# Kernel optimization log

Hardware: AMD Instinct MI355X
Metric: run time of the kernel (lower is better)

Reference implementation:

```python
import jax, jax.numpy as jnp
import numpy as np
from jax import lax

N_FEATURES = 160
HIDDEN = 128
NUM_LAYERS = 2
BATCH = 256
SEQ = 512


def _lstm_layer(x, h0, c0, W_ih, W_hh, b_ih, b_hh):
    """Single LSTM layer, batch_first input x: [B, T, D]. Returns hs: [B, T, H].
    PyTorch gate order: i, f, g, o."""
    b = b_ih + b_hh  # [4H]

    def step(carry, xt):
        h, c = carry
        gates = xt @ W_ih.T + h @ W_hh.T + b  # [B, 4H]
        i, f, g, o = jnp.split(gates, 4, axis=-1)
        i = jax.nn.sigmoid(i)
        f = jax.nn.sigmoid(f)
        g = jnp.tanh(g)
        o = jax.nn.sigmoid(o)
        c = f * c + i * g
        h = o * jnp.tanh(c)
        return (h, c), h

    xs = jnp.swapaxes(x, 0, 1)  # [T, B, D]
    (_, _), hs = lax.scan(step, (h0, c0), xs)
    return jnp.swapaxes(hs, 0, 1)  # [B, T, H]


def setup_inputs() -> dict:
    key = jax.random.key(0)
    ks = jax.random.split(key, 9)
    s = 1.0 / np.sqrt(HIDDEN)  # PyTorch LSTM init scale
    x = jax.random.normal(ks[0], (BATCH, SEQ, N_FEATURES), dtype=jnp.float32)
    h0 = jnp.zeros((NUM_LAYERS, BATCH, HIDDEN), dtype=jnp.float32)
    c0 = jnp.zeros((NUM_LAYERS, BATCH, HIDDEN), dtype=jnp.float32)
    return {
        "x": x,
        "h0": h0,
        "c0": c0,
        "W_ih0": jax.random.uniform(ks[1], (4 * HIDDEN, N_FEATURES), jnp.float32, -s, s),
        "W_hh0": jax.random.uniform(ks[2], (4 * HIDDEN, HIDDEN), jnp.float32, -s, s),
        "b_ih0": jax.random.uniform(ks[3], (4 * HIDDEN,), jnp.float32, -s, s),
        "b_hh0": jax.random.uniform(ks[4], (4 * HIDDEN,), jnp.float32, -s, s),
        "W_ih1": jax.random.uniform(ks[5], (4 * HIDDEN, HIDDEN), jnp.float32, -s, s),
        "W_hh1": jax.random.uniform(ks[6], (4 * HIDDEN, HIDDEN), jnp.float32, -s, s),
        "b_ih1": jax.random.uniform(ks[7], (4 * HIDDEN,), jnp.float32, -s, s),
        "b_hh1": jax.random.uniform(ks[8], (4 * HIDDEN,), jnp.float32, -s, s),
    }


def reference(x, h0, c0, W_ih0, W_hh0, b_ih0, b_hh0, W_ih1, W_hh1, b_ih1, b_hh1):
    h1 = _lstm_layer(x, h0[0], c0[0], W_ih0, W_hh0, b_ih0, b_hh0)   # [B, T, H]
    h2 = _lstm_layer(h1, h0[1], c0[1], W_ih1, W_hh1, b_ih1, b_hh1)  # [B, T, H]
    return h2[:, -1:, :]  # [B, 1, H]
```

## Files before the change

kernel.cpp:

```cpp
#include <hip/hip_runtime.h>


typedef _Float16 half2_t __attribute__((ext_vector_type(2)));

#define TSTEPS 512
#define HID 128

static __device__ __forceinline__ unsigned pack2(float a, float b) {
  half2_t h; h[0] = (_Float16)a; h[1] = (_Float16)b;
  return __builtin_bit_cast(unsigned, h);
}

static __device__ __forceinline__ float dot2f(unsigned a, unsigned b, float c) {
#if __has_builtin(__builtin_amdgcn_fdot2)
  return __builtin_amdgcn_fdot2(__builtin_bit_cast(half2_t, a),
                                __builtin_bit_cast(half2_t, b), c, false);
#else
  half2_t x = __builtin_bit_cast(half2_t, a);
  half2_t y = __builtin_bit_cast(half2_t, b);
  float r = c;
  r = fmaf((float)x[0], (float)y[0], r);
  r = fmaf((float)x[1], (float)y[1], r);
  return r;
#endif
}

static __device__ __forceinline__ float fast_rcp(float x) {
#if __has_builtin(__builtin_amdgcn_rcpf)
  return __builtin_amdgcn_rcpf(x);
#else
  return 1.0f / x;
#endif
}
static __device__ __forceinline__ float fast_exp2(float x) {
#if __has_builtin(__builtin_amdgcn_exp2f)
  return __builtin_amdgcn_exp2f(x);
#else
  return exp2f(x);
#endif
}
static __device__ __forceinline__ float sigm(float x) {
  return fast_rcp(1.0f + fast_exp2(x * -1.44269504f));
}
static __device__ __forceinline__ float tanh_f(float x) {
  float e = fast_exp2(x * 2.885390082f);
  return 1.0f - 2.0f * fast_rcp(e + 1.0f);
}

template <int CTRL>
static __device__ __forceinline__ float qp_add(float v) {
  int iv = __builtin_bit_cast(int, v);
  int t = __builtin_amdgcn_update_dpp(iv, iv, CTRL, 0xF, 0xF, true);
  return v + __builtin_bit_cast(float, t);
}

__global__ __launch_bounds__(512) __attribute__((amdgpu_waves_per_eu(1, 1)))
void lstm_fused(
    const float* __restrict__ x,
    const float* __restrict__ h0,
    const float* __restrict__ c0,
    const float* __restrict__ Wih0,
    const float* __restrict__ Whh0,
    const float* __restrict__ bih0, const float* __restrict__ bhh0,
    const float* __restrict__ Wih1,
    const float* __restrict__ Whh1,
    const float* __restrict__ bih1, const float* __restrict__ bhh1,
    float* __restrict__ out)
{
  const int b   = blockIdx.x;
  const int tid = threadIdx.x;
  const int c   = tid >> 2;
  const int s   = tid & 3;

  __shared__ unsigned h1s[TSTEPS][64];
  __shared__ unsigned xbuf[2][80];
  __shared__ unsigned h0buf[64];
  __shared__ unsigned hbuf[2][64];

  {
    unsigned wx[4][20], wh[4][16];
    float bias[4];
#pragma unroll
    for (int g = 0; g < 4; ++g) {
      const int r = g * HID + c;
#pragma unroll
      for (int j = 0; j < 20; ++j) {
        int p = 20 * s + j;
        wx[g][j] = pack2(Wih0[r * 160 + 2 * p], Wih0[r * 160 + 2 * p + 1]);
      }
#pragma unroll
      for (int j = 0; j < 16; ++j) {
        int p = 16 * s + j;
        wh[g][j] = pack2(Whh0[r * HID + 2 * p], Whh0[r * HID + 2 * p + 1]);
      }
      bias[g] = bih0[r] + bhh0[r];
    }

    float cst = c0[b * HID + c];

    if (tid < 64) h0buf[tid] = pack2(h0[b * HID + 2 * tid], h0[b * HID + 2 * tid + 1]);
    if (tid < 80) {
      float2 v = *(const float2*)&x[((size_t)b * TSTEPS + 0) * 160 + 2 * tid];
      xbuf[0][tid] = pack2(v.x, v.y);
    }
    float2 xA = make_float2(0.f, 0.f);
    if (tid < 80) xA = *(const float2*)&x[((size_t)b * TSTEPS + 1) * 160 + 2 * tid];
    __syncthreads();

#pragma unroll 1
    for (int t = 0; t < TSTEPS; ++t) {
      float2 xB = xA;
      if (tid < 80) {
        int tn = (t + 2 < TSTEPS) ? t + 2 : TSTEPS - 1;
        xB = *(const float2*)&x[((size_t)b * TSTEPS + tn) * 160 + 2 * tid];
      }

      const uint4* xs = (const uint4*)&xbuf[t & 1][20 * s];
      const uint4* hs = (t == 0) ? (const uint4*)&h0buf[16 * s]
                                 : (const uint4*)&h1s[t - 1][16 * s];
      float ai = 0.f, af = 0.f, ag = 0.f, ao = 0.f;
#pragma unroll
      for (int k = 0; k < 5; ++k) {
        uint4 v = xs[k];
        ai = dot2f(v.x, wx[0][4 * k + 0], ai); ai = dot2f(v.y, wx[0][4 * k + 1], ai);
        ai = dot2f(v.z, wx[0][4 * k + 2], ai); ai = dot2f(v.w, wx[0][4 * k + 3], ai);
        af = dot2f(v.x, wx[1][4 * k + 0], af); af = dot2f(v.y, wx[1][4 * k + 1], af);
        af = dot2f(v.z, wx[1][4 * k + 2], af); af = dot2f(v.w, wx[1][4 * k + 3], af);
        ag = dot2f(v.x, wx[2][4 * k + 0], ag); ag = dot2f(v.y, wx[2][4 * k + 1], ag);
        ag = dot2f(v.z, wx[2][4 * k + 2], ag); ag = dot2f(v.w, wx[2][4 * k + 3], ag);
        ao = dot2f(v.x, wx[3][4 * k + 0], ao); ao = dot2f(v.y, wx[3][4 * k + 1], ao);
        ao = dot2f(v.z, wx[3][4 * k + 2], ao); ao = dot2f(v.w, wx[3][4 * k + 3], ao);
      }
#pragma unroll
      for (int k = 0; k < 4; ++k) {
        uint4 v = hs[k];
        ai = dot2f(v.x, wh[0][4 * k + 0], ai); ai = dot2f(v.y, wh[0][4 * k + 1], ai);
        ai = dot2f(v.z, wh[0][4 * k + 2], ai); ai = dot2f(v.w, wh[0][4 * k + 3], ai);
        af = dot2f(v.x, wh[1][4 * k + 0], af); af = dot2f(v.y, wh[1][4 * k + 1], af);
        af = dot2f(v.z, wh[1][4 * k + 2], af); af = dot2f(v.w, wh[1][4 * k + 3], af);
        ag = dot2f(v.x, wh[2][4 * k + 0], ag); ag = dot2f(v.y, wh[2][4 * k + 1], ag);
        ag = dot2f(v.z, wh[2][4 * k + 2], ag); ag = dot2f(v.w, wh[2][4 * k + 3], ag);
        ao = dot2f(v.x, wh[3][4 * k + 0], ao); ao = dot2f(v.y, wh[3][4 * k + 1], ao);
        ao = dot2f(v.z, wh[3][4 * k + 2], ao); ao = dot2f(v.w, wh[3][4 * k + 3], ao);
      }
      ai = qp_add<0xB1>(ai); ai = qp_add<0x4E>(ai);
      af = qp_add<0xB1>(af); af = qp_add<0x4E>(af);
      ag = qp_add<0xB1>(ag); ag = qp_add<0x4E>(ag);
      ao = qp_add<0xB1>(ao); ao = qp_add<0x4E>(ao);

      float iv = sigm(ai + bias[0]);
      float fv = sigm(af + bias[1]);
      float gv = tanh_f(ag + bias[2]);
      float ov = sigm(ao + bias[3]);
      cst = fv * cst + iv * gv;
      float h = ov * tanh_f(cst);

      if (s == 0) ((_Float16*)h1s)[t * HID + c] = (_Float16)h;
      if (tid < 80) xbuf[(t + 1) & 1][tid] = pack2(xA.x, xA.y);
      __syncthreads();
      xA = xB;
    }
  }

  {
    unsigned w1x[4][16], w1h[4][16];
    float bias[4];
#pragma unroll
    for (int g = 0; g < 4; ++g) {
      const int r = g * HID + c;
#pragma unroll
      for (int j = 0; j < 16; ++j) {
        int p = 16 * s + j;
        w1x[g][j] = pack2(Wih1[r * HID + 2 * p], Wih1[r * HID + 2 * p + 1]);
        w1h[g][j] = pack2(Whh1[r * HID + 2 * p], Whh1[r * HID + 2 * p + 1]);
      }
      bias[g] = bih1[r] + bhh1[r];
    }

    const float* h0b = h0 + 256 * HID;
    const float* c0b = c0 + 256 * HID;
    float cst = c0b[b * HID + c];
    if (tid < 64) hbuf[0][tid] = pack2(h0b[b * HID + 2 * tid], h0b[b * HID + 2 * tid + 1]);
    __syncthreads();

    float hlast = 0.f;
#pragma unroll 1
    for (int t = 0; t < TSTEPS; ++t) {
      const uint4* xs = (const uint4*)&h1s[t][16 * s];
      const uint4* hs = (const uint4*)&hbuf[t & 1][16 * s];
      float ai = 0.f, af = 0.f, ag = 0.f, ao = 0.f;
#pragma unroll
      for (int k = 0; k < 4; ++k) {
        uint4 v = xs[k];
        ai = dot2f(v.x, w1x[0][4 * k + 0], ai); ai = dot2f(v.y, w1x[0][4 * k + 1], ai);
        ai = dot2f(v.z, w1x[0][4 * k + 2], ai); ai = dot2f(v.w, w1x[0][4 * k + 3], ai);
        af = dot2f(v.x, w1x[1][4 * k + 0], af); af = dot2f(v.y, w1x[1][4 * k + 1], af);
        af = dot2f(v.z, w1x[1][4 * k + 2], af); af = dot2f(v.w, w1x[1][4 * k + 3], af);
        ag = dot2f(v.x, w1x[2][4 * k + 0], ag); ag = dot2f(v.y, w1x[2][4 * k + 1], ag);
        ag = dot2f(v.z, w1x[2][4 * k + 2], ag); ag = dot2f(v.w, w1x[2][4 * k + 3], ag);
        ao = dot2f(v.x, w1x[3][4 * k + 0], ao); ao = dot2f(v.y, w1x[3][4 * k + 1], ao);
        ao = dot2f(v.z, w1x[3][4 * k + 2], ao); ao = dot2f(v.w, w1x[3][4 * k + 3], ao);
      }
#pragma unroll
      for (int k = 0; k < 4; ++k) {
        uint4 v = hs[k];
        ai = dot2f(v.x, w1h[0][4 * k + 0], ai); ai = dot2f(v.y, w1h[0][4 * k + 1], ai);
        ai = dot2f(v.z, w1h[0][4 * k + 2], ai); ai = dot2f(v.w, w1h[0][4 * k + 3], ai);
        af = dot2f(v.x, w1h[1][4 * k + 0], af); af = dot2f(v.y, w1h[1][4 * k + 1], af);
        af = dot2f(v.z, w1h[1][4 * k + 2], af); af = dot2f(v.w, w1h[1][4 * k + 3], af);
        ag = dot2f(v.x, w1h[2][4 * k + 0], ag); ag = dot2f(v.y, w1h[2][4 * k + 1], ag);
        ag = dot2f(v.z, w1h[2][4 * k + 2], ag); ag = dot2f(v.w, w1h[2][4 * k + 3], ag);
        ao = dot2f(v.x, w1h[3][4 * k + 0], ao); ao = dot2f(v.y, w1h[3][4 * k + 1], ao);
        ao = dot2f(v.z, w1h[3][4 * k + 2], ao); ao = dot2f(v.w, w1h[3][4 * k + 3], ao);
      }
      ai = qp_add<0xB1>(ai); ai = qp_add<0x4E>(ai);
      af = qp_add<0xB1>(af); af = qp_add<0x4E>(af);
      ag = qp_add<0xB1>(ag); ag = qp_add<0x4E>(ag);
      ao = qp_add<0xB1>(ao); ao = qp_add<0x4E>(ao);

      float iv = sigm(ai + bias[0]);
      float fv = sigm(af + bias[1]);
      float gv = tanh_f(ag + bias[2]);
      float ov = sigm(ao + bias[3]);
      cst = fv * cst + iv * gv;
      float h = ov * tanh_f(cst);
      hlast = h;

      if (s == 0) ((_Float16*)&hbuf[(t + 1) & 1][0])[c] = (_Float16)h;
      __syncthreads();
    }
    if (s == 0) out[b * HID + c] = hlast;
  }
}

extern "C" void kernel_launch(void* const* d_in, const int* in_sizes, int n_in,
                              void* d_out, int out_size, void* d_ws,
                              size_t ws_size, hipStream_t stream) {
  const float* x    = (const float*)d_in[0];
  const float* h0   = (const float*)d_in[1];
  const float* c0   = (const float*)d_in[2];
  const float* Wih0 = (const float*)d_in[3];
  const float* Whh0 = (const float*)d_in[4];
  const float* bih0 = (const float*)d_in[5];
  const float* bhh0 = (const float*)d_in[6];
  const float* Wih1 = (const float*)d_in[7];
  const float* Whh1 = (const float*)d_in[8];
  const float* bih1 = (const float*)d_in[9];
  const float* bhh1 = (const float*)d_in[10];

  lstm_fused<<<256, 512, 0, stream>>>(x, h0, c0, Wih0, Whh0, bih0, bhh0,
                                      Wih1, Whh1, bih1, bhh1, (float*)d_out);
}
```

Before: 871.9 us.

## Hoist input projections into MFMA GEMMs and split recurrence into chunked kernels

```diff
diff --git a/kernel.cpp b/kernel.cpp
--- a/kernel.cpp
+++ b/kernel.cpp
@@ -1,16 +1,23 @@
 #include <hip/hip_runtime.h>
 
 
+typedef _Float16 f16;
+typedef _Float16 f16x8 __attribute__((ext_vector_type(8)));
+typedef float f32x4 __attribute__((ext_vector_type(4)));
+
+#define B_  256
+#define T_  512
+#define HID 128
+#define NG  512
+#define KX0 160
+
+static __device__ __forceinline__ unsigned pack2(float a, float b) {
+  union { f16 h[2]; unsigned u; } v;
+  v.h[0] = (f16)a; v.h[1] = (f16)b;
+  return v.u;
+}
+
 typedef _Float16 half2_t __attribute__((ext_vector_type(2)));
-
-#define TSTEPS 512
-#define HID 128
-
-static __device__ __forceinline__ unsigned pack2(float a, float b) {
-  half2_t h; h[0] = (_Float16)a; h[1] = (_Float16)b;
-  return __builtin_bit_cast(unsigned, h);
-}
-
 static __device__ __forceinline__ float dot2f(unsigned a, unsigned b, float c) {
 #if __has_builtin(__builtin_amdgcn_fdot2)
   return __builtin_amdgcn_fdot2(__builtin_bit_cast(half2_t, a),
@@ -54,182 +61,160 @@
   return v + __builtin_bit_cast(float, t);
 }
 
-__global__ __launch_bounds__(512) __attribute__((amdgpu_waves_per_eu(1, 1)))
-void lstm_fused(
-    const float* __restrict__ x,
-    const float* __restrict__ h0,
-    const float* __restrict__ c0,
-    const float* __restrict__ Wih0,
-    const float* __restrict__ Whh0,
-    const float* __restrict__ bih0, const float* __restrict__ bhh0,
-    const float* __restrict__ Wih1,
-    const float* __restrict__ Whh1,
-    const float* __restrict__ bih1, const float* __restrict__ bhh1,
-    float* __restrict__ out)
-{
-  const int b   = blockIdx.x;
+template <int K, bool AF16>
+__global__ __launch_bounds__(256) void gemm_xw(
+    const void* __restrict__ Aptr, size_t bStride, int tcShift, int tcMask,
+    const float* __restrict__ W, f16* __restrict__ D) {
+  constexpr int KP = K + 8;
+  __shared__ f16 As[128][KP];
+  __shared__ f16 Bs[64][KP];
   const int tid = threadIdx.x;
-  const int c   = tid >> 2;
-  const int s   = tid & 3;
-
-  __shared__ unsigned h1s[TSTEPS][64];
-  __shared__ unsigned xbuf[2][80];
-  __shared__ unsigned h0buf[64];
+  const int mtile = blockIdx.x, ntile = blockIdx.y;
+
+  if (AF16) {
+    const f16* A = (const f16*)Aptr;
+    for (int i = tid; i < 128 * (K / 8); i += 256) {
+      int r = i / (K / 8), kk = (i % (K / 8)) * 8;
+      size_t grow = (size_t)mtile * 128 + r;
+      uint4 v = *(const uint4*)(A + grow * K + kk);
+      *(uint4*)&As[r][kk] = v;
+    }
+  } else {
+    const float* A = (const float*)Aptr;
+    for (int i = tid; i < 128 * (K / 4); i += 256) {
+      int r = i / (K / 4), kk = (i % (K / 4)) * 4;
+      int grow = mtile * 128 + r;
+      int bb = grow >> tcShift, tt = grow & tcMask;
+      const float* p = A + (size_t)bb * bStride + (size_t)tt * K + kk;
+      float4 v = *(const float4*)p;
+      uint2 u;
+      u.x = pack2(v.x, v.y);
+      u.y = pack2(v.z, v.w);
+      *(uint2*)&As[r][kk] = u;
+    }
+  }
+  for (int i = tid; i < 64 * (K / 4); i += 256) {
+    int r = i / (K / 4), kk = (i % (K / 4)) * 4;
+    const float* p = W + (size_t)(ntile * 64 + r) * K + kk;
+    float4 v = *(const float4*)p;
+    uint2 u;
+    u.x = pack2(v.x, v.y);
+    u.y = pack2(v.z, v.w);
+    *(uint2*)&Bs[r][kk] = u;
+  }
+  __syncthreads();
+
+  const int w = tid >> 6, l = tid & 63;
+  const int lr = l & 15, lg = l >> 4;
+  f32x4 acc[2][4] = {};
+#pragma unroll
+  for (int ks = 0; ks < K / 32; ++ks) {
+    f16x8 a0 = *(const f16x8*)&As[w * 32 + lr][ks * 32 + lg * 8];
+    f16x8 a1 = *(const f16x8*)&As[w * 32 + 16 + lr][ks * 32 + lg * 8];
+    f16x8 bf[4];
+#pragma unroll
+    for (int nj = 0; nj < 4; ++nj)
+      bf[nj] = *(const f16x8*)&Bs[nj * 16 + lr][ks * 32 + lg * 8];
+#pragma unroll
+    for (int nj = 0; nj < 4; ++nj) {
+      acc[0][nj] = __builtin_amdgcn_mfma_f32_16x16x32_f16(a0, bf[nj], acc[0][nj], 0, 0, 0);
+      acc[1][nj] = __builtin_amdgcn_mfma_f32_16x16x32_f16(a1, bf[nj], acc[1][nj], 0, 0, 0);
+    }
+  }
+#pragma unroll
+  for (int mi = 0; mi < 2; ++mi) {
+#pragma unroll
+    for (int nj = 0; nj < 4; ++nj) {
+      int col = ntile * 64 + nj * 16 + lr;
+#pragma unroll
+      for (int q = 0; q < 4; ++q) {
+        size_t grow = (size_t)mtile * 128 + w * 32 + mi * 16 + lg * 4 + q;
+        D[grow * NG + col] = (f16)acc[mi][nj][q];
+      }
+    }
+  }
+}
+
+__global__ __launch_bounds__(512) void lstm_rec(
+    const f16* __restrict__ Gx,
+    const float* __restrict__ Whh,
+    const float* __restrict__ bih, const float* __restrict__ bhh,
+    const float* __restrict__ hin,
+    const float* __restrict__ cin,
+    float* __restrict__ hstate, float* __restrict__ cstate,
+    f16* __restrict__ h1out,
+    float* __restrict__ finalOut,
+    int Tc) {
+  const int b = blockIdx.x, tid = threadIdx.x;
+  const int c = tid >> 2, s = tid & 3;
   __shared__ unsigned hbuf[2][64];
 
-  {
-    unsigned wx[4][20], wh[4][16];
-    float bias[4];
-#pragma unroll
-    for (int g = 0; g < 4; ++g) {
-      const int r = g * HID + c;
-#pragma unroll
-      for (int j = 0; j < 20; ++j) {
-        int p = 20 * s + j;
-        wx[g][j] = pack2(Wih0[r * 160 + 2 * p], Wih0[r * 160 + 2 * p + 1]);
-      }
-#pragma unroll
-      for (int j = 0; j < 16; ++j) {
-        int p = 16 * s + j;
-        wh[g][j] = pack2(Whh0[r * HID + 2 * p], Whh0[r * HID + 2 * p + 1]);
-      }
-      bias[g] = bih0[r] + bhh0[r];
-    }
-
-    float cst = c0[b * HID + c];
-
-    if (tid < 64) h0buf[tid] = pack2(h0[b * HID + 2 * tid], h0[b * HID + 2 * tid + 1]);
-    if (tid < 80) {
-      float2 v = *(const float2*)&x[((size_t)b * TSTEPS + 0) * 160 + 2 * tid];
-      xbuf[0][tid] = pack2(v.x, v.y);
-    }
-    float2 xA = make_float2(0.f, 0.f);
-    if (tid < 80) xA = *(const float2*)&x[((size_t)b * TSTEPS + 1) * 160 + 2 * tid];
+  unsigned wh[4][16];
+  float bias[4];
+#pragma unroll
+  for (int g = 0; g < 4; ++g) {
+    const int r = g * HID + c;
+#pragma unroll
+    for (int j = 0; j < 16; ++j) {
+      int p = 16 * s + j;
+      wh[g][j] = pack2(Whh[(size_t)r * HID + 2 * p], Whh[(size_t)r * HID + 2 * p + 1]);
+    }
+    bias[g] = bih[r] + bhh[r];
+  }
+  float cst = cin[b * HID + c];
+  if (tid < 64) hbuf[0][tid] = pack2(hin[b * HID + 2 * tid], hin[b * HID + 2 * tid + 1]);
+
+  const f16* gxb = Gx + (size_t)b * Tc * NG;
+  f16 gxc[4], gxn[4];
+#pragma unroll
+  for (int g = 0; g < 4; ++g) gxc[g] = gxb[g * HID + c];
+  __syncthreads();
+
+  float h = 0.f;
+#pragma unroll 1
+  for (int t = 0; t < Tc; ++t) {
+    if (t + 1 < Tc) {
+#pragma unroll
+      for (int g = 0; g < 4; ++g) gxn[g] = gxb[(size_t)(t + 1) * NG + g * HID + c];
+    }
+    const uint4* hs = (const uint4*)&hbuf[t & 1][16 * s];
+    float ai = 0.f, af = 0.f, ag = 0.f, ao = 0.f;
+#pragma unroll
+    for (int k = 0; k < 4; ++k) {
+      uint4 v = hs[k];
+      ai = dot2f(v.x, wh[0][4 * k + 0], ai); ai = dot2f(v.y, wh[0][4 * k + 1], ai);
+      ai = dot2f(v.z, wh[0][4 * k + 2], ai); ai = dot2f(v.w, wh[0][4 * k + 3], ai);
+      af = dot2f(v.x, wh[1][4 * k + 0], af); af = dot2f(v.y, wh[1][4 * k + 1], af);
+      af = dot2f(v.z, wh[1][4 * k + 2], af); af = dot2f(v.w, wh[1][4 * k + 3], af);
+      ag = dot2f(v.x, wh[2][4 * k + 0], ag); ag = dot2f(v.y, wh[2][4 * k + 1], ag);
+      ag = dot2f(v.z, wh[2][4 * k + 2], ag); ag = dot2f(v.w, wh[2][4 * k + 3], ag);
+      ao = dot2f(v.x, wh[3][4 * k + 0], ao); ao = dot2f(v.y, wh[3][4 * k + 1], ao);
+      ao = dot2f(v.z, wh[3][4 * k + 2], ao); ao = dot2f(v.w, wh[3][4 * k + 3], ao);
+    }
+    ai = qp_add<0xB1>(ai); ai = qp_add<0x4E>(ai);
+    af = qp_add<0xB1>(af); af = qp_add<0x4E>(af);
+    ag = qp_add<0xB1>(ag); ag = qp_add<0x4E>(ag);
+    ao = qp_add<0xB1>(ao); ao = qp_add<0x4E>(ao);
+
+    float iv = sigm(ai + bias[0] + (float)gxc[0]);
+    float fv = sigm(af + bias[1] + (float)gxc[1]);
+    float gv = tanh_f(ag + bias[2] + (float)gxc[2]);
+    float ov = sigm(ao + bias[3] + (float)gxc[3]);
+    cst = fv * cst + iv * gv;
+    h = ov * tanh_f(cst);
+    f16 hf = (f16)h;
+    if (s == 0) {
+      ((f16*)&hbuf[(t + 1) & 1][0])[c] = hf;
+      if (h1out) h1out[((size_t)b * Tc + t) * HID + c] = hf;
+    }
     __syncthreads();
-
-#pragma unroll 1
-    for (int t = 0; t < TSTEPS; ++t) {
-      float2 xB = xA;
-      if (tid < 80) {
-        int tn = (t + 2 < TSTEPS) ? t + 2 : TSTEPS - 1;
-        xB = *(const float2*)&x[((size_t)b * TSTEPS + tn) * 160 + 2 * tid];
-      }
-
-      const uint4* xs = (const uint4*)&xbuf[t & 1][20 * s];
-      const uint4* hs = (t == 0) ? (const uint4*)&h0buf[16 * s]
-                                 : (const uint4*)&h1s[t - 1][16 * s];
-      float ai = 0.f, af = 0.f, ag = 0.f, ao = 0.f;
-#pragma unroll
-      for (int k = 0; k < 5; ++k) {
-        uint4 v = xs[k];
-        ai = dot2f(v.x, wx[0][4 * k + 0], ai); ai = dot2f(v.y, wx[0][4 * k + 1], ai);
-        ai = dot2f(v.z, wx[0][4 * k + 2], ai); ai = dot2f(v.w, wx[0][4 * k + 3], ai);
-        af = dot2f(v.x, wx[1][4 * k + 0], af); af = dot2f(v.y, wx[1][4 * k + 1], af);
-        af = dot2f(v.z, wx[1][4 * k + 2], af); af = dot2f(v.w, wx[1][4 * k + 3], af);
-        ag = dot2f(v.x, wx[2][4 * k + 0], ag); ag = dot2f(v.y, wx[2][4 * k + 1], ag);
-        ag = dot2f(v.z, wx[2][4 * k + 2], ag); ag = dot2f(v.w, wx[2][4 * k + 3], ag);
-        ao = dot2f(v.x, wx[3][4 * k + 0], ao); ao = dot2f(v.y, wx[3][4 * k + 1], ao);
-        ao = dot2f(v.z, wx[3][4 * k + 2], ao); ao = dot2f(v.w, wx[3][4 * k + 3], ao);
-      }
-#pragma unroll
-      for (int k = 0; k < 4; ++k) {
-        uint4 v = hs[k];
-        ai = dot2f(v.x, wh[0][4 * k + 0], ai); ai = dot2f(v.y, wh[0][4 * k + 1], ai);
-        ai = dot2f(v.z, wh[0][4 * k + 2], ai); ai = dot2f(v.w, wh[0][4 * k + 3], ai);
-        af = dot2f(v.x, wh[1][4 * k + 0], af); af = dot2f(v.y, wh[1][4 * k + 1], af);
-        af = dot2f(v.z, wh[1][4 * k + 2], af); af = dot2f(v.w, wh[1][4 * k + 3], af);
-        ag = dot2f(v.x, wh[2][4 * k + 0], ag); ag = dot2f(v.y, wh[2][4 * k + 1], ag);
-        ag = dot2f(v.z, wh[2][4 * k + 2], ag); ag = dot2f(v.w, wh[2][4 * k + 3], ag);
-        ao = dot2f(v.x, wh[3][4 * k + 0], ao); ao = dot2f(v.y, wh[3][4 * k + 1], ao);
-        ao = dot2f(v.z, wh[3][4 * k + 2], ao); ao = dot2f(v.w, wh[3][4 * k + 3], ao);
-      }
-      ai = qp_add<0xB1>(ai); ai = qp_add<0x4E>(ai);
-      af = qp_add<0xB1>(af); af = qp_add<0x4E>(af);
-      ag = qp_add<0xB1>(ag); ag = qp_add<0x4E>(ag);
-      ao = qp_add<0xB1>(ao); ao = qp_add<0x4E>(ao);
-
-      float iv = sigm(ai + bias[0]);
-      float fv = sigm(af + bias[1]);
-      float gv = tanh_f(ag + bias[2]);
-      float ov = sigm(ao + bias[3]);
-      cst = fv * cst + iv * gv;
-      float h = ov * tanh_f(cst);
-
-      if (s == 0) ((_Float16*)h1s)[t * HID + c] = (_Float16)h;
-      if (tid < 80) xbuf[(t + 1) & 1][tid] = pack2(xA.x, xA.y);
-      __syncthreads();
-      xA = xB;
-    }
-  }
-
-  {
-    unsigned w1x[4][16], w1h[4][16];
-    float bias[4];
-#pragma unroll
-    for (int g = 0; g < 4; ++g) {
-      const int r = g * HID + c;
-#pragma unroll
-      for (int j = 0; j < 16; ++j) {
-        int p = 16 * s + j;
-        w1x[g][j] = pack2(Wih1[r * HID + 2 * p], Wih1[r * HID + 2 * p + 1]);
-        w1h[g][j] = pack2(Whh1[r * HID + 2 * p], Whh1[r * HID + 2 * p + 1]);
-      }
-      bias[g] = bih1[r] + bhh1[r];
-    }
-
-    const float* h0b = h0 + 256 * HID;
-    const float* c0b = c0 + 256 * HID;
-    float cst = c0b[b * HID + c];
-    if (tid < 64) hbuf[0][tid] = pack2(h0b[b * HID + 2 * tid], h0b[b * HID + 2 * tid + 1]);
-    __syncthreads();
-
-    float hlast = 0.f;
-#pragma unroll 1
-    for (int t = 0; t < TSTEPS; ++t) {
-      const uint4* xs = (const uint4*)&h1s[t][16 * s];
-      const uint4* hs = (const uint4*)&hbuf[t & 1][16 * s];
-      float ai = 0.f, af = 0.f, ag = 0.f, ao = 0.f;
-#pragma unroll
-      for (int k = 0; k < 4; ++k) {
-        uint4 v = xs[k];
-        ai = dot2f(v.x, w1x[0][4 * k + 0], ai); ai = dot2f(v.y, w1x[0][4 * k + 1], ai);
-        ai = dot2f(v.z, w1x[0][4 * k + 2], ai); ai = dot2f(v.w, w1x[0][4 * k + 3], ai);
-        af = dot2f(v.x, w1x[1][4 * k + 0], af); af = dot2f(v.y, w1x[1][4 * k + 1], af);
-        af = dot2f(v.z, w1x[1][4 * k + 2], af); af = dot2f(v.w, w1x[1][4 * k + 3], af);
-        ag = dot2f(v.x, w1x[2][4 * k + 0], ag); ag = dot2f(v.y, w1x[2][4 * k + 1], ag);
-        ag = dot2f(v.z, w1x[2][4 * k + 2], ag); ag = dot2f(v.w, w1x[2][4 * k + 3], ag);
-        ao = dot2f(v.x, w1x[3][4 * k + 0], ao); ao = dot2f(v.y, w1x[3][4 * k + 1], ao);
-        ao = dot2f(v.z, w1x[3][4 * k + 2], ao); ao = dot2f(v.w, w1x[3][4 * k + 3], ao);
-      }
-#pragma unroll
-      for (int k = 0; k < 4; ++k) {
-        uint4 v = hs[k];
-        ai = dot2f(v.x, w1h[0][4 * k + 0], ai); ai = dot2f(v.y, w1h[0][4 * k + 1], ai);
-        ai = dot2f(v.z, w1h[0][4 * k + 2], ai); ai = dot2f(v.w, w1h[0][4 * k + 3], ai);
-        af = dot2f(v.x, w1h[1][4 * k + 0], af); af = dot2f(v.y, w1h[1][4 * k + 1], af);
-        af = dot2f(v.z, w1h[1][4 * k + 2], af); af = dot2f(v.w, w1h[1][4 * k + 3], af);
-        ag = dot2f(v.x, w1h[2][4 * k + 0], ag); ag = dot2f(v.y, w1h[2][4 * k + 1], ag);
-        ag = dot2f(v.z, w1h[2][4 * k + 2], ag); ag = dot2f(v.w, w1h[2][4 * k + 3], ag);
-        ao = dot2f(v.x, w1h[3][4 * k + 0], ao); ao = dot2f(v.y, w1h[3][4 * k + 1], ao);
-        ao = dot2f(v.z, w1h[3][4 * k + 2], ao); ao = dot2f(v.w, w1h[3][4 * k + 3], ao);
-      }
-      ai = qp_add<0xB1>(ai); ai = qp_add<0x4E>(ai);
-      af = qp_add<0xB1>(af); af = qp_add<0x4E>(af);
-      ag = qp_add<0xB1>(ag); ag = qp_add<0x4E>(ag);
-      ao = qp_add<0xB1>(ao); ao = qp_add<0x4E>(ao);
-
-      float iv = sigm(ai + bias[0]);
-      float fv = sigm(af + bias[1]);
-      float gv = tanh_f(ag + bias[2]);
-      float ov = sigm(ao + bias[3]);
-      cst = fv * cst + iv * gv;
-      float h = ov * tanh_f(cst);
-      hlast = h;
-
-      if (s == 0) ((_Float16*)&hbuf[(t + 1) & 1][0])[c] = (_Float16)h;
-      __syncthreads();
-    }
-    if (s == 0) out[b * HID + c] = hlast;
+#pragma unroll
+    for (int g = 0; g < 4; ++g) gxc[g] = gxn[g];
+  }
+  if (s == 0) {
+    hstate[b * HID + c] = (float)(f16)h;
+    cstate[b * HID + c] = cst;
+    if (finalOut) finalOut[b * HID + c] = h;
   }
 }
 
@@ -248,6 +233,40 @@
   const float* bih1 = (const float*)d_in[9];
   const float* bhh1 = (const float*)d_in[10];
 
-  lstm_fused<<<256, 512, 0, stream>>>(x, h0, c0, Wih0, Whh0, bih0, bhh0,
-                                      Wih1, Whh1, bih1, bhh1, (float*)d_out);
-}
+  int NC = 16;
+  for (int n = 1; n <= 16; n *= 2) {
+    size_t tc = T_ / n;
+    size_t need = (size_t)B_ * tc * NG * 2
+                + (size_t)B_ * tc * HID * 2
+                + 4 * (size_t)B_ * HID * 4
+                + 256;
+    if (need <= ws_size) { NC = n; break; }
+  }
+  const int Tc = T_ / NC;
+  int tcShift = 0;
+  while ((1 << tcShift) < Tc) ++tcShift;
+
+  char* w = (char*)d_ws;
+  f16* Gx = (f16*)w;        w += (size_t)B_ * Tc * NG * 2;
+  f16* h1 = (f16*)w;        w += (size_t)B_ * Tc * HID * 2;
+  float* sH0 = (float*)w;   w += (size_t)B_ * HID * 4;
+  float* sC0 = (float*)w;   w += (size_t)B_ * HID * 4;
+  float* sH1 = (float*)w;   w += (size_t)B_ * HID * 4;
+  float* sC1 = (float*)w;
+
+  const dim3 ggrid(2 * Tc, 8);
+  for (int cc = 0; cc < NC; ++cc) {
+    gemm_xw<KX0, false><<<ggrid, 256, 0, stream>>>(
+        x + (size_t)cc * Tc * KX0, (size_t)T_ * KX0, tcShift, Tc - 1, Wih0, Gx);
+    lstm_rec<<<B_, 512, 0, stream>>>(
+        Gx, Whh0, bih0, bhh0,
+        cc == 0 ? h0 : sH0, cc == 0 ? c0 : sC0, sH0, sC0,
+        h1, nullptr, Tc);
+    gemm_xw<HID, true><<<ggrid, 256, 0, stream>>>(
+        h1, 0, tcShift, Tc - 1, Wih1, Gx);
+    lstm_rec<<<B_, 512, 0, stream>>>(
+        Gx, Whh1, bih1, bhh1,
+        cc == 0 ? h0 + B_ * HID : sH1, cc == 0 ? c0 + B_ * HID : sC1, sH1, sC1,
+        nullptr, cc == NC - 1 ? (float*)d_out : nullptr, Tc);
+  }
+}
```

Result: slower. 1.110 ms (+27.3%).
